# Kernel tuning notes

Hardware: AMD Instinct MI355X
Metric: run time of the kernel (lower is better)

The kernel has to match this reference:

```python
import jax, jax.numpy as jnp
import numpy as np
from jax import lax

HEADS = 8  # num_heads; also must equal cols of the input

def _conv_same(x, W, b):
    # x: (N, C_in, H, W), W: (C_out, C_in, kh, kw) -- Conv2d with padding='same'
    y = lax.conv_general_dilated(x, W, (1, 1), 'SAME',
                                 dimension_numbers=('NCHW', 'OIHW', 'NCHW'))
    return y + b[None, :, None, None]

def setup_inputs() -> dict:
    key = jax.random.key(0)
    ks = jax.random.split(key, 11)
    B, S, D, R, C = 4, 8, 512, 32, 8  # cols C == num_heads (required by the reshape)
    f = 3
    inp = {
        'q': jax.random.normal(ks[0], (B, S, D, R, C), jnp.float32),
        'k': jax.random.normal(ks[1], (B, S, D, R, C), jnp.float32),
        'v': jax.random.normal(ks[2], (B, S, D, R, C), jnp.float32),
        'Wq': jax.random.normal(ks[3], (D, D, f, f), jnp.float32) * 0.02,
        'bq': jnp.zeros((D,), jnp.float32),
        'Wk': jax.random.normal(ks[4], (D, D, f, f), jnp.float32) * 0.02,
        'bk': jnp.zeros((D,), jnp.float32),
        'Wv': jax.random.normal(ks[5], (D, D, f, f), jnp.float32) * 0.02,
        'bv': jnp.zeros((D,), jnp.float32),
        'Wo': jax.random.normal(ks[6], (D, D, f, f), jnp.float32) * 0.02,
        'bo': jnp.zeros((D,), jnp.float32),
    }
    return inp

def reference(q, k, v, Wq, bq, Wk, bk, Wv, bv, Wo, bo):
    B, S, D, R, C = q.shape
    H = HEADS
    dep = C // H  # = 1 with C == H (attention 'depth' per the original view math)

    def proj_split(x, W, b):
        y = _conv_same(x.reshape(B * S, D, R, C), W, b)          # (N, D, R, C)
        y = y.reshape(1, H, B * S, D, R, C // H)                  # raw view as in torch
        return y.transpose(0, 2, 3, 4, 1, 5)                      # (1, N, D, R, H, dep)

    q6 = proj_split(q, Wq, bq)
    k6 = proj_split(k, Wk, bk)
    v6 = proj_split(v, Wv, bv)

    # vectorized form of the per-step loop: dot over (rows, H, dep), softmax over keys
    scores = jnp.einsum('bnqrhd,bnkrhd->bnqk', q6, k6) / jnp.sqrt(jnp.float32(dep))
    attn = jax.nn.softmax(scores, axis=-1)                        # (1, N, D, D)
    out = jnp.einsum('bnqk,bnkrhd->bnqrhd', attn, v6)             # (1, N, D, R, H, dep)

    sa = out.reshape(B, S, R, H, D).transpose(0, 4, 1, 2, 3)      # (B, D, S, R, H)
    y = _conv_same(sa.reshape(B, D, S, R * H), Wo, bo)            # channels = d_model
    y = y.reshape(B, D, S, R, H)
    return y, attn
```

## Files before the change

### kernel.cpp

```cpp
#include <hip/hip_runtime.h>


typedef __attribute__((ext_vector_type(8))) short short8;
typedef __attribute__((ext_vector_type(8))) _Float16 half8;
typedef __attribute__((ext_vector_type(4))) float f32x4;
typedef __attribute__((ext_vector_type(4))) short short4v;

#define MFMA16F(a, b, c) __builtin_amdgcn_mfma_f32_16x16x32_f16((a), (b), (c), 0, 0, 0)

__device__ __forceinline__ void gl_lds16(const void* g, void* l) {
    __builtin_amdgcn_global_load_lds(
        (const __attribute__((address_space(1))) unsigned int*)g,
        (__attribute__((address_space(3))) unsigned int*)l, 16, 0, 0);
}
__device__ __forceinline__ unsigned short f2h(float f) {
    _Float16 h = (_Float16)f;
    return __builtin_bit_cast(unsigned short, h);
}

__global__ __launch_bounds__(256) void k_prep_fused(
        const float* __restrict__ q, const float* __restrict__ k,
        const float* __restrict__ v,
        const float* __restrict__ Wq, const float* __restrict__ Wk,
        const float* __restrict__ Wv, const float* __restrict__ Wo,
        unsigned short* __restrict__ Wqh, unsigned short* __restrict__ Wkh,
        unsigned short* __restrict__ Wvh, unsigned short* __restrict__ Woh,
        unsigned short* __restrict__ Xqh, unsigned short* __restrict__ Xkh,
        unsigned short* __restrict__ Xvh) {
    __shared__ __align__(16) unsigned int U[8192];
    const int b = blockIdx.x;
    const int tid = threadIdx.x;
    if (b < 1536) {
        const int cig = b & 15, n = (b >> 4) & 31, z = b >> 9;
        const float* X = z == 0 ? q : z == 1 ? k : v;
        unsigned short* Xh = z == 0 ? Xqh : z == 1 ? Xkh : Xvh;
#pragma unroll
        for (int it = 0; it < 8; ++it) {
            int ci_l = it * 4 + (tid >> 6);
            int pos = (tid & 63) * 4;
            const float4 rd =
                *(const float4*)&X[(size_t)(n * 512 + cig * 32 + ci_l) * 256 + pos];
            uint4 u;
            u.x = f2h(rd.x);
            u.y = f2h(rd.y);
            u.z = f2h(rd.z);
            u.w = f2h(rd.w);
            *(uint4*)&U[ci_l * 256 + pos] = u;
        }
        __syncthreads();
#pragma unroll
        for (int it = 0; it < 4; ++it) {
            int pos = it * 64 + (tid >> 2);
            int ci8 = (tid & 3) * 8;
            short8 h8;
#pragma unroll
            for (int j = 0; j < 8; ++j)
                h8[j] = (short)(U[(ci8 + j) * 256 + pos] & 0xffffu);
            int yy = (pos >> 3) + 1, xx = (pos & 7) + 1;
            size_t o = (size_t)((n * 34 + yy) * 10 + xx) * 512 + cig * 32 + ci8;
            *(short8*)&Xh[o] = h8;
        }
    } else if (b < 3584) {
        const int bl = b - 1536;
        const int co = bl & 511, z = bl >> 9;
        const float* W = z == 0 ? Wq : z == 1 ? Wk : z == 2 ? Wv : Wo;
        unsigned short* Wh = z == 0 ? Wqh : z == 1 ? Wkh : z == 2 ? Wvh : Woh;
        const float* Wc = W + co * 4608;
#pragma unroll
        for (int it = 0; it < 9; ++it) {
            int p = it * 256 + tid;
            float2 rd = *(const float2*)&Wc[p * 2];
            int e0 = p * 2;
            int ci0 = e0 / 9, t0 = e0 - ci0 * 9;
            U[t0 * 512 + ci0] = f2h(rd.x);
            int e1 = e0 + 1;
            int ci1 = e1 / 9, t1 = e1 - ci1 * 9;
            U[t1 * 512 + ci1] = f2h(rd.y);
        }
        __syncthreads();
        unsigned short* Whc = Wh + co * 4608;
#pragma unroll
        for (int it = 0; it < 18; ++it) {
            int j = it * 256 + tid;
            Whc[j] = (unsigned short)U[j];
        }
    } else {
        const int w = tid >> 6, l = tid & 63;
        int job = (b - 3584) * 4 + w;
        int a = job / 2688;
        int r = job - a * 2688;
        int n = r / 84;
        int ii = r - n * 84;
        unsigned short* arr = a == 0 ? Xqh : a == 1 ? Xkh : Xvh;
        int cell;
        if (ii < 11)      cell = ii;
        else if (ii < 73) { int j = ii - 11; cell = 19 + (j >> 1) * 10 + (j & 1); }
        else              cell = 329 + (ii - 73);
        short8 z8 = {0, 0, 0, 0, 0, 0, 0, 0};
        *(short8*)&arr[(size_t)(n * 340 + cell) * 512 + l * 8] = z8;
    }
}

__global__ __launch_bounds__(256) void k_conv_qkv_all(
        const unsigned short* __restrict__ Xqh, const unsigned short* __restrict__ Xkh,
        const unsigned short* __restrict__ Xvh,
        const unsigned short* __restrict__ Wqh_, const unsigned short* __restrict__ Wkh_,
        const unsigned short* __restrict__ Wvh_,
        const float* __restrict__ bq, const float* __restrict__ bk,
        const float* __restrict__ bv,
        unsigned short* __restrict__ Qh, unsigned short* __restrict__ Kh,
        unsigned short* __restrict__ Vt) {
    __shared__ __align__(16) short Ah[8192], Bh[8192];
    const int z = blockIdx.z;
    const unsigned short* Xh = z == 0 ? Xqh : z == 1 ? Xkh : Xvh;
    const unsigned short* Wh = z == 0 ? Wqh_ : z == 1 ? Wkh_ : Wvh_;
    const float* bias = z == 0 ? bq : z == 1 ? bk : bv;

    const int tid = threadIdx.x;
    const int w = tid >> 6, l = tid & 63;
    const int n   = blockIdx.x >> 1;
    const int p0  = (blockIdx.x & 1) * 128;
    const int co0 = blockIdx.y * 128;
    const int lm = l & 15, lq = l >> 4;
    const int r8 = l >> 3, c8 = (l & 7) ^ (l >> 3);

    int arow[4], brow[4];
#pragma unroll
    for (int j = 0; j < 4; ++j) {
        int rt = w * 32 + j * 8 + r8;
        int px = p0 + rt;
        int y = px >> 3, x = px & 7;
        arow[j] = ((n * 34 + y + 1) * 10 + (x + 1)) * 512 + c8 * 8;
        brow[j] = (co0 + rt) * 4608 + c8 * 8;
    }
    const int ldsW = w * 4096;

    int aoff[4][2], boff[4][2];
#pragma unroll
    for (int mi = 0; mi < 4; ++mi) {
        int row = (w & 1) * 64 + mi * 16 + lm;
#pragma unroll
        for (int ks = 0; ks < 2; ++ks)
            aoff[mi][ks] = row * 64 + ((((ks << 2) | lq) ^ (row & 7)) * 8);
    }
#pragma unroll
    for (int ni = 0; ni < 4; ++ni) {
        int row = (w >> 1) * 64 + ni * 16 + lm;
#pragma unroll
        for (int ks = 0; ks < 2; ++ks)
            boff[ni][ks] = row * 64 + ((((ks << 2) | lq) ^ (row & 7)) * 8);
    }

    f32x4 acc[4][4];
#pragma unroll
    for (int ni = 0; ni < 4; ++ni) {
        float b = bias[co0 + (w >> 1) * 64 + ni * 16 + lm];
#pragma unroll
        for (int mi = 0; mi < 4; ++mi) acc[mi][ni] = (f32x4){b, b, b, b};
    }

    for (int tap = 0; tap < 9; ++tap) {
        const int tapoff = ((tap / 3 - 1) * 10 + (tap % 3 - 1)) * 512;
        const int wb = tap * 512;
        for (int ci0 = 0; ci0 < 512; ci0 += 64) {
#pragma unroll
            for (int j = 0; j < 4; ++j)
                gl_lds16(Xh + arow[j] + tapoff + ci0, (char*)Ah + ldsW + j * 1024);
#pragma unroll
            for (int j = 0; j < 4; ++j)
                gl_lds16(Wh + brow[j] + wb + ci0, (char*)Bh + ldsW + j * 1024);
            __syncthreads();
            __builtin_amdgcn_s_setprio(1);
#pragma unroll
            for (int ks = 0; ks < 2; ++ks) {
                half8 ah[4], bh[4];
#pragma unroll
                for (int mi = 0; mi < 4; ++mi)
                    ah[mi] = *(const half8*)&Ah[aoff[mi][ks]];
#pragma unroll
                for (int ni = 0; ni < 4; ++ni)
                    bh[ni] = *(const half8*)&Bh[boff[ni][ks]];
#pragma unroll
                for (int mi = 0; mi < 4; ++mi)
#pragma unroll
                    for (int ni = 0; ni < 4; ++ni)
                        acc[mi][ni] = MFMA16F(ah[mi], bh[ni], acc[mi][ni]);
            }
            __builtin_amdgcn_s_setprio(0);
            __syncthreads();
        }
    }

    const int hh = n >> 2, nl = n & 3;
    const int pxbase = p0 + (w & 1) * 64 + lq * 4;
    const int x0q = pxbase & 7;
#pragma unroll
    for (int mi = 0; mi < 4; ++mi) {
        int px = pxbase + mi * 16;
        int y = px >> 3;
#pragma unroll
        for (int ni = 0; ni < 4; ++ni) {
            int co = co0 + (w >> 1) * 64 + ni * 16 + lm;
            int nn = nl * 8 + (co >> 6);
            int dd = (co & 63) * 8 + (y >> 2);
            int t0 = hh * 32 + (y & 3) * 8 + x0q;
            if (z < 2) {
                unsigned short* O = (z == 0) ? Qh : Kh;
                short4v hv;
#pragma unroll
                for (int r = 0; r < 4; ++r) hv[r] = (short)f2h(acc[mi][ni][r]);
                *(short4v*)&O[(nn * 512 + dd) * 256 + t0] = hv;
            } else {
#pragma unroll
                for (int r = 0; r < 4; ++r)
                    Vt[(nn * 256 + t0 + r) * 512 + dd] = f2h(acc[mi][ni][r]);
            }
        }
    }
}

__global__ __launch_bounds__(256) void k_scores_mfma(
        const unsigned short* __restrict__ Qh, const unsigned short* __restrict__ Kh,
        float* __restrict__ Sc) {
    __shared__ __align__(16) short Ah[16384], Bh[16384];
    const int tid = threadIdx.x;
    const int w = tid >> 6, l = tid & 63;
    const int q0 = blockIdx.x * 128, k0 = blockIdx.y * 128, nn = blockIdx.z;
    const int lm = l & 15, lq = l >> 4;
    const int r4 = l >> 4, c16 = l & 15;

    int arow[8], brow[8];
#pragma unroll
    for (int j = 0; j < 8; ++j) {
        int rt = w * 32 + j * 4 + r4;
        int sw = (c16 ^ (rt & 15)) * 8;
        arow[j] = (nn * 512 + q0 + rt) * 256 + sw;
        brow[j] = (nn * 512 + k0 + rt) * 256 + sw;
    }
    const int ldsW = w * 8192;

    int aoff[4][4], boff[4][4];
#pragma unroll
    for (int mi = 0; mi < 4; ++mi) {
        int row = (w & 1) * 64 + mi * 16 + lm;
#pragma unroll
        for (int ks = 0; ks < 4; ++ks)
            aoff[mi][ks] = row * 128 + ((((ks << 2) | lq) ^ (row & 15)) * 8);
    }
#pragma unroll
    for (int ni = 0; ni < 4; ++ni) {
        int row = (w >> 1) * 64 + ni * 16 + lm;
#pragma unroll
        for (int ks = 0; ks < 4; ++ks)
            boff[ni][ks] = row * 128 + ((((ks << 2) | lq) ^ (row & 15)) * 8);
    }

    f32x4 acc[4][4];
#pragma unroll
    for (int mi = 0; mi < 4; ++mi)
#pragma unroll
        for (int ni = 0; ni < 4; ++ni) acc[mi][ni] = (f32x4){0.f, 0.f, 0.f, 0.f};

    for (int t0 = 0; t0 < 256; t0 += 128) {
#pragma unroll
        for (int j = 0; j < 8; ++j)
            gl_lds16(Qh + arow[j] + t0, (char*)Ah + ldsW + j * 1024);
#pragma unroll
        for (int j = 0; j < 8; ++j)
            gl_lds16(Kh + brow[j] + t0, (char*)Bh + ldsW + j * 1024);
        __syncthreads();
#pragma unroll
        for (int ks = 0; ks < 4; ++ks) {
            half8 ah[4], bh[4];
#pragma unroll
            for (int mi = 0; mi < 4; ++mi) ah[mi] = *(const half8*)&Ah[aoff[mi][ks]];
#pragma unroll
            for (int ni = 0; ni < 4; ++ni) bh[ni] = *(const half8*)&Bh[boff[ni][ks]];
#pragma unroll
            for (int mi = 0; mi < 4; ++mi)
#pragma unroll
                for (int ni = 0; ni < 4; ++ni)
                    acc[mi][ni] = MFMA16F(ah[mi], bh[ni], acc[mi][ni]);
        }
        __syncthreads();
    }

    float* C = Sc + nn * 262144;
#pragma unroll
    for (int mi = 0; mi < 4; ++mi) {
        int qb = q0 + (w & 1) * 64 + lq * 4 + mi * 16;
#pragma unroll
        for (int ni = 0; ni < 4; ++ni) {
            int col = k0 + (w >> 1) * 64 + ni * 16 + lm;
#pragma unroll
            for (int r = 0; r < 4; ++r)
                C[(qb + r) * 512 + col] = acc[mi][ni][r];
        }
    }
}

__global__ __launch_bounds__(256) void k_softmax(float* __restrict__ Sc,
                                                 unsigned short* __restrict__ Ph,
                                                 unsigned int* __restrict__ Spz) {
    unsigned base = blockIdx.x * 256 + threadIdx.x;
#pragma unroll
    for (int i = 0; i < 3; ++i) {
        unsigned zi = base + (unsigned)i * 1048576u;
        if (zi < 2641920u) Spz[zi] = 0u;
    }
    const int w = threadIdx.x >> 6, l = threadIdx.x & 63;
    float* p = Sc + ((size_t)blockIdx.x * 4 + w) * 512;
    unsigned short* ph = Ph + ((size_t)blockIdx.x * 4 + w) * 512;
    const int i0 = l * 4, i1 = 256 + l * 4;
    float4 a = *(const float4*)&p[i0];
    float4 b = *(const float4*)&p[i1];
    float m = fmaxf(fmaxf(fmaxf(a.x, a.y), fmaxf(a.z, a.w)),
                    fmaxf(fmaxf(b.x, b.y), fmaxf(b.z, b.w)));
#pragma unroll
    for (int off = 32; off; off >>= 1) m = fmaxf(m, __shfl_xor(m, off));
    float e0 = __expf(a.x - m), e1 = __expf(a.y - m);
    float e2 = __expf(a.z - m), e3 = __expf(a.w - m);
    float e4 = __expf(b.x - m), e5 = __expf(b.y - m);
    float e6 = __expf(b.z - m), e7 = __expf(b.w - m);
    float s = ((e0 + e1) + (e2 + e3)) + ((e4 + e5) + (e6 + e7));
#pragma unroll
    for (int off = 32; off; off >>= 1) s += __shfl_xor(s, off);
    float inv = 1.0f / s;
    float4 o0 = {e0 * inv, e1 * inv, e2 * inv, e3 * inv};
    float4 o1 = {e4 * inv, e5 * inv, e6 * inv, e7 * inv};
    *(float4*)&p[i0] = o0;
    *(float4*)&p[i1] = o1;
    short4v h0 = {(short)f2h(o0.x), (short)f2h(o0.y), (short)f2h(o0.z), (short)f2h(o0.w)};
    short4v h1 = {(short)f2h(o1.x), (short)f2h(o1.y), (short)f2h(o1.z), (short)f2h(o1.w)};
    *(short4v*)&ph[i0] = h0;
    *(short4v*)&ph[i1] = h1;
}

__global__ __launch_bounds__(256) void k_pv_mfma(
        const unsigned short* __restrict__ Ph, const unsigned short* __restrict__ Vt,
        unsigned short* __restrict__ Sp) {
    __shared__ __align__(16) short Ah[16384], Bh[8192];
    const int tid = threadIdx.x;
    const int w = tid >> 6, l = tid & 63;
    const int q0 = blockIdx.x * 128, t0 = blockIdx.y * 64, nn = blockIdx.z;
    const int lm = l & 15, lq = l >> 4;
    const int r4 = l >> 4, c16 = l & 15;

    int arow[8], brow[4];
#pragma unroll
    for (int j = 0; j < 8; ++j) {
        int rt = w * 32 + j * 4 + r4;
        arow[j] = (nn * 512 + q0 + rt) * 512 + ((c16 ^ (rt & 15)) * 8);
    }
#pragma unroll
    for (int j = 0; j < 4; ++j) {
        int rt = w * 16 + j * 4 + r4;
        brow[j] = (nn * 256 + t0 + rt) * 512 + ((c16 ^ (rt & 15)) * 8);
    }
    const int ldsA = w * 8192, ldsB = w * 4096;

    int aoff[4][4], boff[2][4];
#pragma unroll
    for (int mi = 0; mi < 4; ++mi) {
        int row = (w & 1) * 64 + mi * 16 + lm;
#pragma unroll
        for (int ks = 0; ks < 4; ++ks)
            aoff[mi][ks] = row * 128 + ((((ks << 2) | lq) ^ (row & 15)) * 8);
    }
#pragma unroll
    for (int ni = 0; ni < 2; ++ni) {
        int row = (w >> 1) * 32 + ni * 16 + lm;
#pragma unroll
        for (int ks = 0; ks < 4; ++ks)
            boff[ni][ks] = row * 128 + ((((ks << 2) | lq) ^ (row & 15)) * 8);
    }

    f32x4 acc[4][2];
#pragma unroll
    for (int mi = 0; mi < 4; ++mi)
#pragma unroll
        for (int ni = 0; ni < 2; ++ni) acc[mi][ni] = (f32x4){0.f, 0.f, 0.f, 0.f};

    for (int kc = 0; kc < 512; kc += 128) {
#pragma unroll
        for (int j = 0; j < 8; ++j)
            gl_lds16(Ph + arow[j] + kc, (char*)Ah + ldsA + j * 1024);
#pragma unroll
        for (int j = 0; j < 4; ++j)
            gl_lds16(Vt + brow[j] + kc, (char*)Bh + ldsB + j * 1024);
        __syncthreads();
#pragma unroll
        for (int ks = 0; ks < 4; ++ks) {
            half8 a[4], b[2];
#pragma unroll
            for (int mi = 0; mi < 4; ++mi) a[mi] = *(const half8*)&Ah[aoff[mi][ks]];
#pragma unroll
            for (int ni = 0; ni < 2; ++ni) b[ni] = *(const half8*)&Bh[boff[ni][ks]];
#pragma unroll
            for (int mi = 0; mi < 4; ++mi)
#pragma unroll
                for (int ni = 0; ni < 2; ++ni)
                    acc[mi][ni] = MFMA16F(a[mi], b[ni], acc[mi][ni]);
        }
        __syncthreads();
    }

    const int b2 = nn >> 3, s2 = nn & 7;
#pragma unroll
    for (int mi = 0; mi < 4; ++mi) {
        int qb = q0 + (w & 1) * 64 + lq * 4 + mi * 16;
#pragma unroll
        for (int ni = 0; ni < 2; ++ni) {
            int tc = t0 + (w >> 1) * 32 + ni * 16 + lm;
            int d2base = (tc & 31) * 8 + (tc >> 5);
#pragma unroll
            for (int r = 0; r < 4; ++r) {
                int qp = qb + r;
                int ww = (qp >> 4) * 8 + ((qp >> 1) & 7);
                int d2 = (qp & 1) * 256 + d2base;
                Sp[((b2 * 10 + s2 + 1) * 258 + ww + 1) * 512 + d2] =
                    f2h(acc[mi][ni][r]);
            }
        }
    }
}

__global__ __launch_bounds__(256) void k_conv_o_mfma(
        const unsigned short* __restrict__ Sp, const unsigned short* __restrict__ Wh,
        const float* __restrict__ bias, float* __restrict__ Y) {
    __shared__ __align__(16) short Ah[16384], Bh[8192];
    const int tid = threadIdx.x;
    const int w = tid >> 6, l = tid & 63;
    const int n   = blockIdx.x >> 4;
    const int yy  = (blockIdx.x >> 1) & 7;
    const int x0  = (blockIdx.x & 1) * 128;
    const int co0 = blockIdx.y * 64;
    const int lm = l & 15, lq = l >> 4;
    const int r4 = l >> 4, c16 = l & 15;

    int arow[8], brow[4];
#pragma unroll
    for (int j = 0; j < 8; ++j) {
        int rt = w * 32 + j * 4 + r4;
        arow[j] = ((n * 10 + yy + 1) * 258 + (x0 + rt + 1)) * 512
                  + ((c16 ^ (rt & 15)) * 8);
    }
#pragma unroll
    for (int j = 0; j < 4; ++j) {
        int rt = w * 16 + j * 4 + r4;
        brow[j] = (co0 + rt) * 4608 + ((c16 ^ (rt & 15)) * 8);
    }
    const int ldsA = w * 8192, ldsB = w * 4096;

    int aoff[4][4], boff[2][4];
#pragma unroll
    for (int mi = 0; mi < 4; ++mi) {
        int row = (w & 1) * 64 + mi * 16 + lm;
#pragma unroll
        for (int ks = 0; ks < 4; ++ks)
            aoff[mi][ks] = row * 128 + ((((ks << 2) | lq) ^ (row & 15)) * 8);
    }
#pragma unroll
    for (int ni = 0; ni < 2; ++ni) {
        int row = (w >> 1) * 32 + ni * 16 + lm;
#pragma unroll
        for (int ks = 0; ks < 4; ++ks)
            boff[ni][ks] = row * 128 + ((((ks << 2) | lq) ^ (row & 15)) * 8);
    }

    f32x4 acc[4][2];
#pragma unroll
    for (int ni = 0; ni < 2; ++ni) {
        float b = bias[co0 + (w >> 1) * 32 + ni * 16 + lm];
#pragma unroll
        for (int mi = 0; mi < 4; ++mi) acc[mi][ni] = (f32x4){b, b, b, b};
    }

    for (int tap = 0; tap < 9; ++tap) {
        const int tapoff = ((tap / 3 - 1) * 258 + (tap % 3 - 1)) * 512;
        const int wb = tap * 512;
        for (int ci0 = 0; ci0 < 512; ci0 += 128) {
#pragma unroll
            for (int j = 0; j < 8; ++j)
                gl_lds16(Sp + arow[j] + tapoff + ci0, (char*)Ah + ldsA + j * 1024);
#pragma unroll
            for (int j = 0; j < 4; ++j)
                gl_lds16(Wh + brow[j] + wb + ci0, (char*)Bh + ldsB + j * 1024);
            __syncthreads();
#pragma unroll
            for (int ks = 0; ks < 4; ++ks) {
                half8 a[4], b[2];
#pragma unroll
                for (int mi = 0; mi < 4; ++mi)
                    a[mi] = *(const half8*)&Ah[aoff[mi][ks]];
#pragma unroll
                for (int ni = 0; ni < 2; ++ni)
                    b[ni] = *(const half8*)&Bh[boff[ni][ks]];
#pragma unroll
                for (int mi = 0; mi < 4; ++mi)
#pragma unroll
                    for (int ni = 0; ni < 2; ++ni)
                        acc[mi][ni] = MFMA16F(a[mi], b[ni], acc[mi][ni]);
            }
            __syncthreads();
        }
    }

#pragma unroll
    for (int mi = 0; mi < 4; ++mi) {
        int px = x0 + (w & 1) * 64 + lq * 4 + mi * 16;
#pragma unroll
        for (int ni = 0; ni < 2; ++ni) {
            int co = co0 + (w >> 1) * 32 + ni * 16 + lm;
            *(f32x4*)&Y[n * 1048576 + co * 2048 + yy * 256 + px] = acc[mi][ni];
        }
    }
}

extern "C" void kernel_launch(void* const* d_in, const int* in_sizes, int n_in,
                              void* d_out, int out_size, void* d_ws, size_t ws_size,
                              hipStream_t stream) {
    const float* q  = (const float*)d_in[0];
    const float* k  = (const float*)d_in[1];
    const float* v  = (const float*)d_in[2];
    const float* Wq = (const float*)d_in[3];
    const float* bq = (const float*)d_in[4];
    const float* Wk = (const float*)d_in[5];
    const float* bk = (const float*)d_in[6];
    const float* Wv = (const float*)d_in[7];
    const float* bv = (const float*)d_in[8];
    const float* Wo = (const float*)d_in[9];
    const float* bo = (const float*)d_in[10];

    unsigned short* W0  = (unsigned short*)d_ws;
    unsigned short* Wqh = W0;
    unsigned short* Wkh = W0 + 2359296;
    unsigned short* Wvh = W0 + 4718592;
    unsigned short* Xvh = W0 + 7077888;
    unsigned short* Woh = W0 + 18219008;
    unsigned short* Qh  = W0 + 20578304;
    unsigned short* Kh  = W0 + 28966912;
    unsigned short* Vt  = W0 + 33161216;
    unsigned short* Ph = W0;
    unsigned short* Sp = W0 + 20578304;

    float* y_out = (float*)d_out;
    float* attn  = y_out + 4194304;
    unsigned short* Xqh = (unsigned short*)d_out;
    unsigned short* Xkh = (unsigned short*)attn;

    k_prep_fused<<<5600, 256, 0, stream>>>(q, k, v, Wq, Wk, Wv, Wo,
                                           Wqh, Wkh, Wvh, Woh,
                                           Xqh, Xkh, Xvh);
    k_conv_qkv_all<<<dim3(64, 4, 3), 256, 0, stream>>>(
        Xqh, Xkh, Xvh, Wqh, Wkh, Wvh,
        bq, bk, bv, Qh, Kh, Vt);
    k_scores_mfma<<<dim3(4, 4, 32), 256, 0, stream>>>(Qh, Kh, attn);
    k_softmax<<<4096, 256, 0, stream>>>(attn, Ph, (unsigned int*)Sp);
    k_pv_mfma<<<dim3(4, 4, 32), 256, 0, stream>>>(Ph, Vt, Sp);
    k_conv_o_mfma<<<dim3(64, 8), 256, 0, stream>>>(Sp, Woh, bo, y_out);
}
```

Measured before the change: 367.4 us.

## Fuse QK^T scores and row softmax into one full-row MFMA kernel

Replaces the separate scores GEMM and softmax kernels with one kernel where each 512-thread block owns 64 query rows across all 512 keys. The block computes the row max and sum with cross-wave LDS reductions and writes both the fp32 attention and the fp16 P directly. This removes one launch and the fp32 score round-trip through global memory. Zeroing of the Sp buffer moves into this kernel using uint4 stores, and Sp is relocated in the workspace so it no longer aliases Qh. The new tiling launches only 256 blocks and keeps a large 64KB LDS tile of K, which may lower occupancy.

```diff
diff --git a/kernel.cpp b/kernel.cpp
--- a/kernel.cpp
+++ b/kernel.cpp
@@ -219,121 +219,144 @@
     }
 }
 
-__global__ __launch_bounds__(256) void k_scores_mfma(
+__global__ __launch_bounds__(512) void k_scores_sm(
         const unsigned short* __restrict__ Qh, const unsigned short* __restrict__ Kh,
-        float* __restrict__ Sc) {
-    __shared__ __align__(16) short Ah[16384], Bh[16384];
+        float* __restrict__ Sc, unsigned short* __restrict__ Ph,
+        uint4* __restrict__ Spz) {
+    __shared__ __align__(16) short Ah[4096], Bh[32768];
+    __shared__ float Mw[8][64], Sw[8][64];
     const int tid = threadIdx.x;
+    const int nn = blockIdx.y, q0 = blockIdx.x * 64;
+
+    {
+        unsigned g = (blockIdx.y * 8u + blockIdx.x) * 512u + tid;
+#pragma unroll
+        for (int i = 0; i < 6; ++i) {
+            unsigned zi = g + (unsigned)i * 131072u;
+            if (zi < 660480u) Spz[zi] = (uint4){0u, 0u, 0u, 0u};
+        }
+    }
+
     const int w = tid >> 6, l = tid & 63;
-    const int q0 = blockIdx.x * 128, k0 = blockIdx.y * 128, nn = blockIdx.z;
+    const int wq = w & 1, wk = w >> 1;
     const int lm = l & 15, lq = l >> 4;
-    const int r4 = l >> 4, c16 = l & 15;
-
-    int arow[8], brow[8];
-#pragma unroll
-    for (int j = 0; j < 8; ++j) {
-        int rt = w * 32 + j * 4 + r4;
-        int sw = (c16 ^ (rt & 15)) * 8;
-        arow[j] = (nn * 512 + q0 + rt) * 256 + sw;
-        brow[j] = (nn * 512 + k0 + rt) * 256 + sw;
-    }
-    const int ldsW = w * 8192;
-
-    int aoff[4][4], boff[4][4];
-#pragma unroll
-    for (int mi = 0; mi < 4; ++mi) {
-        int row = (w & 1) * 64 + mi * 16 + lm;
-#pragma unroll
-        for (int ks = 0; ks < 4; ++ks)
-            aoff[mi][ks] = row * 128 + ((((ks << 2) | lq) ^ (row & 15)) * 8);
-    }
-#pragma unroll
-    for (int ni = 0; ni < 4; ++ni) {
-        int row = (w >> 1) * 64 + ni * 16 + lm;
-#pragma unroll
-        for (int ks = 0; ks < 4; ++ks)
-            boff[ni][ks] = row * 128 + ((((ks << 2) | lq) ^ (row & 15)) * 8);
-    }
-
-    f32x4 acc[4][4];
-#pragma unroll
-    for (int mi = 0; mi < 4; ++mi)
-#pragma unroll
-        for (int ni = 0; ni < 4; ++ni) acc[mi][ni] = (f32x4){0.f, 0.f, 0.f, 0.f};
-
-    for (int t0 = 0; t0 < 256; t0 += 128) {
-#pragma unroll
-        for (int j = 0; j < 8; ++j)
-            gl_lds16(Qh + arow[j] + t0, (char*)Ah + ldsW + j * 1024);
-#pragma unroll
-        for (int j = 0; j < 8; ++j)
-            gl_lds16(Kh + brow[j] + t0, (char*)Bh + ldsW + j * 1024);
+
+    const int ar = tid >> 3, ac = (tid & 7) ^ ((tid >> 3) & 7);
+    const int arow = (nn * 512 + q0 + ar) * 256 + ac * 8;
+    int brow[8];
+#pragma unroll
+    for (int it = 0; it < 8; ++it) {
+        int u = it * 512 + tid;
+        int row = u >> 3, slot = u & 7;
+        brow[it] = (nn * 512 + row) * 256 + ((slot ^ (row & 7)) * 8);
+    }
+
+    int aoff[2][2], boff[8][2];
+#pragma unroll
+    for (int mi = 0; mi < 2; ++mi) {
+        int row = wq * 32 + mi * 16 + lm;
+#pragma unroll
+        for (int ks = 0; ks < 2; ++ks)
+            aoff[mi][ks] = row * 64 + ((((ks << 2) | lq) ^ (row & 7)) * 8);
+    }
+#pragma unroll
+    for (int ni = 0; ni < 8; ++ni) {
+        int row = wk * 128 + ni * 16 + lm;
+#pragma unroll
+        for (int ks = 0; ks < 2; ++ks)
+            boff[ni][ks] = row * 64 + ((((ks << 2) | lq) ^ (row & 7)) * 8);
+    }
+
+    f32x4 acc[2][8];
+#pragma unroll
+    for (int mi = 0; mi < 2; ++mi)
+#pragma unroll
+        for (int ni = 0; ni < 8; ++ni) acc[mi][ni] = (f32x4){0.f, 0.f, 0.f, 0.f};
+
+    for (int tc = 0; tc < 256; tc += 64) {
+        gl_lds16(Qh + arow + tc, (char*)Ah + (tid >> 3) * 128 + ((tid & 7) ^ ((tid >> 3) & 7)) * 16 - ((tid & 7) ^ ((tid >> 3) & 7)) * 16 + (tid & 7) * 16);
+#pragma unroll
+        for (int it = 0; it < 8; ++it)
+            gl_lds16(Kh + brow[it] + tc, (char*)Bh + (it * 512 + tid) * 16);
         __syncthreads();
-#pragma unroll
-        for (int ks = 0; ks < 4; ++ks) {
-            half8 ah[4], bh[4];
-#pragma unroll
-            for (int mi = 0; mi < 4; ++mi) ah[mi] = *(const half8*)&Ah[aoff[mi][ks]];
-#pragma unroll
-            for (int ni = 0; ni < 4; ++ni) bh[ni] = *(const half8*)&Bh[boff[ni][ks]];
-#pragma unroll
-            for (int mi = 0; mi < 4; ++mi)
-#pragma unroll
-                for (int ni = 0; ni < 4; ++ni)
+        __builtin_amdgcn_s_setprio(1);
+#pragma unroll
+        for (int ks = 0; ks < 2; ++ks) {
+            half8 ah[2], bh[8];
+#pragma unroll
+            for (int mi = 0; mi < 2; ++mi) ah[mi] = *(const half8*)&Ah[aoff[mi][ks]];
+#pragma unroll
+            for (int ni = 0; ni < 8; ++ni) bh[ni] = *(const half8*)&Bh[boff[ni][ks]];
+#pragma unroll
+            for (int mi = 0; mi < 2; ++mi)
+#pragma unroll
+                for (int ni = 0; ni < 8; ++ni)
                     acc[mi][ni] = MFMA16F(ah[mi], bh[ni], acc[mi][ni]);
         }
+        __builtin_amdgcn_s_setprio(0);
         __syncthreads();
     }
 
+    float M[2][4];
+#pragma unroll
+    for (int mi = 0; mi < 2; ++mi)
+#pragma unroll
+        for (int r = 0; r < 4; ++r) {
+            float m = acc[mi][0][r];
+#pragma unroll
+            for (int ni = 1; ni < 8; ++ni) m = fmaxf(m, acc[mi][ni][r]);
+#pragma unroll
+            for (int off = 1; off < 16; off <<= 1) m = fmaxf(m, __shfl_xor(m, off));
+            M[mi][r] = m;
+            if (lm == 0) Mw[w][wq * 32 + mi * 16 + lq * 4 + r] = m;
+        }
+    __syncthreads();
+#pragma unroll
+    for (int mi = 0; mi < 2; ++mi)
+#pragma unroll
+        for (int r = 0; r < 4; ++r) {
+            int q_l = wq * 32 + mi * 16 + lq * 4 + r;
+            float m = fmaxf(fmaxf(Mw[wq][q_l], Mw[wq + 2][q_l]),
+                            fmaxf(Mw[wq + 4][q_l], Mw[wq + 6][q_l]));
+            M[mi][r] = m;
+        }
+    float S[2][4];
+#pragma unroll
+    for (int mi = 0; mi < 2; ++mi)
+#pragma unroll
+        for (int r = 0; r < 4; ++r) {
+            float m = M[mi][r];
+            float s = 0.f;
+#pragma unroll
+            for (int ni = 0; ni < 8; ++ni) {
+                float e = __expf(acc[mi][ni][r] - m);
+                acc[mi][ni][r] = e;
+                s += e;
+            }
+#pragma unroll
+            for (int off = 1; off < 16; off <<= 1) s += __shfl_xor(s, off);
+            S[mi][r] = s;
+            if (lm == 0) Sw[w][wq * 32 + mi * 16 + lq * 4 + r] = s;
+        }
+    __syncthreads();
     float* C = Sc + nn * 262144;
-#pragma unroll
-    for (int mi = 0; mi < 4; ++mi) {
-        int qb = q0 + (w & 1) * 64 + lq * 4 + mi * 16;
-#pragma unroll
-        for (int ni = 0; ni < 4; ++ni) {
-            int col = k0 + (w >> 1) * 64 + ni * 16 + lm;
-#pragma unroll
-            for (int r = 0; r < 4; ++r)
-                C[(qb + r) * 512 + col] = acc[mi][ni][r];
-        }
-    }
-}
-
-__global__ __launch_bounds__(256) void k_softmax(float* __restrict__ Sc,
-                                                 unsigned short* __restrict__ Ph,
-                                                 unsigned int* __restrict__ Spz) {
-    unsigned base = blockIdx.x * 256 + threadIdx.x;
-#pragma unroll
-    for (int i = 0; i < 3; ++i) {
-        unsigned zi = base + (unsigned)i * 1048576u;
-        if (zi < 2641920u) Spz[zi] = 0u;
-    }
-    const int w = threadIdx.x >> 6, l = threadIdx.x & 63;
-    float* p = Sc + ((size_t)blockIdx.x * 4 + w) * 512;
-    unsigned short* ph = Ph + ((size_t)blockIdx.x * 4 + w) * 512;
-    const int i0 = l * 4, i1 = 256 + l * 4;
-    float4 a = *(const float4*)&p[i0];
-    float4 b = *(const float4*)&p[i1];
-    float m = fmaxf(fmaxf(fmaxf(a.x, a.y), fmaxf(a.z, a.w)),
-                    fmaxf(fmaxf(b.x, b.y), fmaxf(b.z, b.w)));
-#pragma unroll
-    for (int off = 32; off; off >>= 1) m = fmaxf(m, __shfl_xor(m, off));
-    float e0 = __expf(a.x - m), e1 = __expf(a.y - m);
-    float e2 = __expf(a.z - m), e3 = __expf(a.w - m);
-    float e4 = __expf(b.x - m), e5 = __expf(b.y - m);
-    float e6 = __expf(b.z - m), e7 = __expf(b.w - m);
-    float s = ((e0 + e1) + (e2 + e3)) + ((e4 + e5) + (e6 + e7));
-#pragma unroll
-    for (int off = 32; off; off >>= 1) s += __shfl_xor(s, off);
-    float inv = 1.0f / s;
-    float4 o0 = {e0 * inv, e1 * inv, e2 * inv, e3 * inv};
-    float4 o1 = {e4 * inv, e5 * inv, e6 * inv, e7 * inv};
-    *(float4*)&p[i0] = o0;
-    *(float4*)&p[i1] = o1;
-    short4v h0 = {(short)f2h(o0.x), (short)f2h(o0.y), (short)f2h(o0.z), (short)f2h(o0.w)};
-    short4v h1 = {(short)f2h(o1.x), (short)f2h(o1.y), (short)f2h(o1.z), (short)f2h(o1.w)};
-    *(short4v*)&ph[i0] = h0;
-    *(short4v*)&ph[i1] = h1;
+    unsigned short* P = Ph + nn * 262144;
+#pragma unroll
+    for (int mi = 0; mi < 2; ++mi)
+#pragma unroll
+        for (int r = 0; r < 4; ++r) {
+            int q_l = wq * 32 + mi * 16 + lq * 4 + r;
+            float s = ((Sw[wq][q_l] + Sw[wq + 2][q_l]) +
+                       (Sw[wq + 4][q_l] + Sw[wq + 6][q_l]));
+            float inv = 1.0f / s;
+            int rowbase = (q0 + q_l) * 512 + wk * 128 + lm;
+#pragma unroll
+            for (int ni = 0; ni < 8; ++ni) {
+                float p = acc[mi][ni][r] * inv;
+                C[rowbase + ni * 16] = p;
+                P[rowbase + ni * 16] = f2h(p);
+            }
+        }
 }
 
 __global__ __launch_bounds__(256) void k_pv_mfma(
@@ -537,12 +560,12 @@
     unsigned short* Wkh = W0 + 2359296;
     unsigned short* Wvh = W0 + 4718592;
     unsigned short* Xvh = W0 + 7077888;
+    unsigned short* Sp  = W0 + 12648448;
     unsigned short* Woh = W0 + 18219008;
     unsigned short* Qh  = W0 + 20578304;
     unsigned short* Kh  = W0 + 28966912;
     unsigned short* Vt  = W0 + 33161216;
     unsigned short* Ph = W0;
-    unsigned short* Sp = W0 + 20578304;
 
     float* y_out = (float*)d_out;
     float* attn  = y_out + 4194304;
@@ -555,8 +578,7 @@
     k_conv_qkv_all<<<dim3(64, 4, 3), 256, 0, stream>>>(
         Xqh, Xkh, Xvh, Wqh, Wkh, Wvh,
         bq, bk, bv, Qh, Kh, Vt);
-    k_scores_mfma<<<dim3(4, 4, 32), 256, 0, stream>>>(Qh, Kh, attn);
-    k_softmax<<<4096, 256, 0, stream>>>(attn, Ph, (unsigned int*)Sp);
+    k_scores_sm<<<dim3(8, 32), 512, 0, stream>>>(Qh, Kh, attn, Ph, (uint4*)Sp);
     k_pv_mfma<<<dim3(4, 4, 32), 256, 0, stream>>>(Ph, Vt, Sp);
     k_conv_o_mfma<<<dim3(64, 8), 256, 0, stream>>>(Sp, Woh, bo, y_out);
 }
```

Result: no change. 362.2 us (-1.4%).
